# Optimization experiments

Hardware: AMD Instinct MI355X
Metric: run time of the kernel (lower is better)

## Reference

```python
import jax, jax.numpy as jnp
import numpy as np

N, E = 100000, 1600000
IN, H, OUT = 64, 64, 32
BN_EPS = 1e-5


def setup_inputs() -> dict:
    key = jax.random.key(0)
    ks = jax.random.split(key, 13)

    def w(k, shape, fan_in):
        return jax.random.uniform(k, shape, jnp.float32, -1.0, 1.0) / np.sqrt(fan_in)

    return {
        "x": jax.random.normal(ks[0], (N, IN), jnp.float32),
        "edge_index": jax.random.randint(ks[1], (2, E), 0, N, jnp.int32),
        "W1": w(ks[2], (IN, H), IN),
        "b1": jnp.zeros((H,), jnp.float32),
        "gamma": jnp.ones((H,), jnp.float32),
        "beta": jnp.zeros((H,), jnp.float32),
        "W2": w(ks[3], (H, H), H),
        "b2": jnp.zeros((H,), jnp.float32),
        "lin2_w": w(ks[4], (H, OUT), H),
        "lin2_b": w(ks[5], (OUT,), H),
        "lin3_w": w(ks[6], (OUT, H), OUT),
        "lin3_b": w(ks[7], (H,), OUT),
    }


def gcn_conv(x, src, dst, W, b):
    # PyG GCNConv: h = D^{-1/2} (A + I) D^{-1/2} (x W) + b
    n = x.shape[0]
    h = x @ W  # [N, H]
    loop = jnp.arange(n, dtype=src.dtype)
    s = jnp.concatenate([src, loop])  # add self-loops
    d = jnp.concatenate([dst, loop])
    deg = jax.ops.segment_sum(jnp.ones_like(s, x.dtype), d, num_segments=n)
    dinv = jnp.where(deg > 0, jax.lax.rsqrt(deg), 0.0)
    norm = dinv[s] * dinv[d]  # [E+N]
    msg = h[s] * norm[:, None]  # gather + scale
    out = jax.ops.segment_sum(msg, d, num_segments=n)  # scatter-add
    return out + b


def reference(x, edge_index, W1, b1, gamma, beta, W2, b2, lin2_w, lin2_b, lin3_w, lin3_b):
    src, dst = edge_index[0], edge_index[1]
    h = gcn_conv(x, src, dst, W1, b1)
    # BatchNorm1d in eval mode with default running stats (mean=0, var=1)
    h = gamma * (h * jax.lax.rsqrt(jnp.float32(1.0 + BN_EPS))) + beta
    h = jax.nn.relu(h)  # dropout is identity in eval
    h = gcn_conv(h, src, dst, W2, b2)
    logits = h @ lin2_w + lin2_b  # [N, OUT]
    p = jax.nn.softmax(logits, axis=-1)
    ent = -jnp.sum(p * jnp.log(p + 1e-9), axis=-1)  # [N]
    wts = 1.0 / (ent + 1e-10)
    wts = (wts - wts.min()) / (wts.max() - wts.min())
    wts = jax.nn.softmax(wts, axis=0)  # [N]
    graph = jnp.sum(logits * wts[:, None], axis=0, keepdims=True)  # [1, OUT]
    return graph @ lin3_w + lin3_b  # [1, H]
```

## Files before the change

### kernel.cpp

```cpp
#include <hip/hip_runtime.h>
#include <hip/hip_bf16.h>
#include <hip/hip_fp8.h>
#include <math.h>


#define F 64
#define OUTF 32
#define PB 128
#define LEDGE 5632
#define WG 512
#define BN_INV 0.9999950000374997f
#define ESC_X 32.0f
#define IESC_X 0.03125f
#define ESC_Z 64.0f
#define IESC_Z 0.015625f

typedef short bf16x8 __attribute__((ext_vector_type(8)));
typedef float f32x4 __attribute__((ext_vector_type(4)));

__device__ __forceinline__ unsigned short f2bf(float f) {
    unsigned u = __float_as_uint(f);
    return (unsigned short)((u + 0x7fffu + ((u >> 16) & 1u)) >> 16);
}
__device__ __forceinline__ float bf2f(unsigned short h) {
    return __uint_as_float((unsigned)h << 16);
}

#if __has_builtin(__builtin_amdgcn_cvt_f32_fp8) && __has_builtin(__builtin_amdgcn_cvt_pk_fp8_f32)
__device__ __forceinline__ float4 fp8x4(unsigned v) {
    return make_float4(__builtin_amdgcn_cvt_f32_fp8((int)v, 0),
                       __builtin_amdgcn_cvt_f32_fp8((int)v, 1),
                       __builtin_amdgcn_cvt_f32_fp8((int)v, 2),
                       __builtin_amdgcn_cvt_f32_fp8((int)v, 3));
}
__device__ __forceinline__ unsigned fp8pk4(float a, float b, float c, float d) {
    int r = __builtin_amdgcn_cvt_pk_fp8_f32(a, b, 0, false);
    r = __builtin_amdgcn_cvt_pk_fp8_f32(c, d, r, true);
    return (unsigned)r;
}
__device__ __forceinline__ unsigned char fp8enc1(float a) {
    return (unsigned char)(__builtin_amdgcn_cvt_pk_fp8_f32(a, a, 0, false) & 0xff);
}
#else
__device__ __forceinline__ float fp8d1(unsigned char b) {
    __hip_fp8_e4m3 v; v.__x = (__hip_fp8_storage_t)b; return (float)v;
}
__device__ __forceinline__ float4 fp8x4(unsigned v) {
    return make_float4(fp8d1(v & 255u), fp8d1((v >> 8) & 255u), fp8d1((v >> 16) & 255u), fp8d1((v >> 24) & 255u));
}
__device__ __forceinline__ unsigned char fp8enc1(float a) {
    return (unsigned char)__hip_fp8_e4m3(a).__x;
}
__device__ __forceinline__ unsigned fp8pk4(float a, float b, float c, float d) {
    return (unsigned)fp8enc1(a) | ((unsigned)fp8enc1(b) << 8) | ((unsigned)fp8enc1(c) << 16) | ((unsigned)fp8enc1(d) << 24);
}
#endif

__global__ __launch_bounds__(256) void k_hist(const int* __restrict__ dst, int* __restrict__ hist,
                                              int E, int NBK,
                                              const float* __restrict__ W1, const float* __restrict__ b1,
                                              const float* __restrict__ gamma, const float* __restrict__ beta,
                                              const float* __restrict__ W2, const float* __restrict__ b2,
                                              const float* __restrict__ l2w, const float* __restrict__ l2b,
                                              unsigned short* __restrict__ w1f, unsigned short* __restrict__ w2f,
                                              float* __restrict__ bias1f, float* __restrict__ b2l2) {
    __shared__ int lh[512];
    int t = threadIdx.x, blk = blockIdx.x;
    if (blk >= PB) {
        int tt = (blk - PB) * 256 + t;
        int k = tt >> 5, cc = tt & 31;
        float o = 0.0f;
        for (int j = 0; j < F; j++) o += W2[k * F + j] * l2w[j * OUTF + cc];
        {
            int t2 = cc >> 4, s = k >> 5, kb = (k >> 3) & 3, jj = k & 7;
            int ln = kb * 16 + (cc & 15);
            w2f[(size_t)((t2 * 2 + s) * 64 + ln) * 8 + jj] = f2bf(o);
        }
        for (int e = tt; e < F * F; e += 2048) {
            int kk = e >> 6, c = e & 63;
            float wv = W1[kk * F + c] * gamma[c] * BN_INV;
            int t1i = c >> 4, s = kk >> 5, kb = (kk >> 3) & 3, jj = kk & 7;
            int ln = kb * 16 + (c & 15);
            w1f[(size_t)((t1i * 2 + s) * 64 + ln) * 8 + jj] = f2bf(wv);
        }
        if (tt < F) bias1f[tt] = fmaf(b1[tt], gamma[tt] * BN_INV, beta[tt]);
        if (tt < OUTF) {
            float b = l2b[tt];
            for (int j = 0; j < F; j++) b += b2[j] * l2w[j * OUTF + tt];
            b2l2[tt] = b;
        }
        return;
    }
    for (int b = t; b < NBK; b += 256) lh[b] = 0;
    __syncthreads();
    int chunk = (E + PB - 1) / PB;
    int beg = blk * chunk, end = min(beg + chunk, E);
    for (int e = beg + t; e < end; e += 256) atomicAdd(&lh[dst[e] >> 8], 1);
    __syncthreads();
    for (int b = t; b < NBK; b += 256) hist[blk * NBK + b] = lh[b];
}

__global__ __launch_bounds__(PB) void k_hscan1(int* __restrict__ hist, int* __restrict__ btot, int NBK) {
    __shared__ int s[PB];
    int b = blockIdx.x, t = threadIdx.x;
    int v = hist[t * NBK + b];
    s[t] = v;
    __syncthreads();
    for (int off = 1; off < PB; off <<= 1) {
        int u = (t >= off) ? s[t - off] : 0;
        __syncthreads();
        s[t] += u;
        __syncthreads();
    }
    hist[t * NBK + b] = s[t] - v;
    if (t == PB - 1) btot[b] = s[t];
}

__global__ void k_hscan2(const int* __restrict__ btot, int* __restrict__ bbase, int NBK) {
    __shared__ int s[512];
    int t = threadIdx.x;
    int v = (t < NBK) ? btot[t] : 0;
    s[t] = v;
    __syncthreads();
    for (int off = 1; off < 512; off <<= 1) {
        int u = (t >= off) ? s[t - off] : 0;
        __syncthreads();
        s[t] += u;
        __syncthreads();
    }
    if (t < NBK) {
        bbase[t] = s[t] - v;
        if (t == NBK - 1) bbase[NBK] = s[t];
    }
}

__global__ __launch_bounds__(256) void k_place(const int* __restrict__ src, const int* __restrict__ dst,
                                               const int* __restrict__ hist, const int* __restrict__ bbase,
                                               unsigned* __restrict__ bucketArr, int E, int NBK) {
    __shared__ int cur[512];
    int t = threadIdx.x, blk = blockIdx.x;
    for (int b = t; b < NBK; b += 256) cur[b] = hist[blk * NBK + b] + bbase[b];
    __syncthreads();
    int chunk = (E + PB - 1) / PB;
    int beg = blk * chunk, end = min(beg + chunk, E);
    for (int e = beg + t; e < end; e += 256) {
        int d = dst[e], sidx = src[e];
        int p = atomicAdd(&cur[d >> 8], 1);
        bucketArr[p] = ((unsigned)sidx << 8) | (unsigned)(d & 255);
    }
}

__global__ __launch_bounds__(256) void k_binsort(const unsigned* __restrict__ bucketArr,
                                                 const int* __restrict__ bbase,
                                                 int* __restrict__ eidx, int4* __restrict__ meta,
                                                 const float4* __restrict__ x4, unsigned* __restrict__ xq, int N) {
    __shared__ unsigned ledge[LEDGE];
    __shared__ int lcnt[256], lofs[256], lcur[256], lscan[256];
    __shared__ float ldinv[256];
    int b = blockIdx.x, t = threadIdx.x;
    int gb = bbase[b];
    int count = min(bbase[b + 1] - gb, LEDGE);
    for (int j = t; j < count; j += 256) ledge[j] = bucketArr[gb + j];
    lcnt[t] = 0;
    __syncthreads();
    for (int j = t; j < count; j += 256) atomicAdd(&lcnt[ledge[j] & 255u], 1);
    __syncthreads();
    int deg = lcnt[t];
    lscan[t] = deg;
    __syncthreads();
    for (int off = 1; off < 256; off <<= 1) {
        int u = (t >= off) ? lscan[t - off] : 0;
        __syncthreads();
        lscan[t] += u;
        __syncthreads();
    }
    lofs[t] = lscan[t] - deg;
    lcur[t] = 0;
    int node = (b << 8) + t;
    float di = rsqrtf((float)deg + 1.0f);
    ldinv[t] = di;
    if (node < N) meta[node] = make_int4(gb + lofs[t], deg, __float_as_int(di), 0);
    __syncthreads();
    for (int j = t; j < count; j += 256) {
        unsigned v = ledge[j];
        int loc = (int)(v & 255u);
        int p = atomicAdd(&lcur[loc], 1);
        eidx[gb + lofs[loc] + p] = (int)(v >> 8);
    }
    for (int idx = t; idx < 256 * 16; idx += 256) {
        int nd = (b << 8) + (idx >> 4);
        if (nd < N) {
            float d2 = ldinv[idx >> 4] * ESC_X;
            float4 v = x4[(size_t)nd * 16 + (idx & 15)];
            xq[(size_t)nd * 16 + (idx & 15)] = fp8pk4(v.x * d2, v.y * d2, v.z * d2, v.w * d2);
        }
    }
}

__device__ __forceinline__ void conv1_consume(const uint2 (&vbuf)[24], uint2 selfv, int dcnt,
                                              int i, int beg, float dis, int gl, int gbase,
                                              const uint2* __restrict__ xq2, const int* __restrict__ eidx,
                                              int Em1, unsigned short* __restrict__ t1, int N) {
    float4 aA0 = fp8x4(selfv.x), aB0 = fp8x4(selfv.y);
    float4 aA1 = make_float4(0.f, 0.f, 0.f, 0.f), aB1 = aA1;
#pragma unroll
    for (int k = 0; k < 24; k++) {
        if (k < dcnt) {
            float4 vA = fp8x4(vbuf[k].x), vB = fp8x4(vbuf[k].y);
            if (k & 1) {
                aA1.x += vA.x; aA1.y += vA.y; aA1.z += vA.z; aA1.w += vA.w;
                aB1.x += vB.x; aB1.y += vB.y; aB1.z += vB.z; aB1.w += vB.w;
            } else {
                aA0.x += vA.x; aA0.y += vA.y; aA0.z += vA.z; aA0.w += vA.w;
                aB0.x += vB.x; aB0.y += vB.y; aB0.z += vB.z; aB0.w += vB.w;
            }
        }
    }
    for (int base = 24; base < dcnt; base += 8) {
        int j = base + gl;
        int ss = eidx[min(beg + j, Em1)];
        int cnt = min(dcnt - base, 8);
#pragma unroll
        for (int k = 0; k < 8; k++) {
            if (k < cnt) {
                int sv = __shfl(ss, gbase + k, 64);
                uint2 v = xq2[(size_t)sv * 8 + gl];
                float4 vA = fp8x4(v.x), vB = fp8x4(v.y);
                aA0.x += vA.x; aA0.y += vA.y; aA0.z += vA.z; aA0.w += vA.w;
                aB0.x += vB.x; aB0.y += vB.y; aB0.z += vB.z; aB0.w += vB.w;
            }
        }
    }
    if (i < N) {
        float4 oA, oB;
        oA.x = (aA0.x + aA1.x) * dis; oA.y = (aA0.y + aA1.y) * dis;
        oA.z = (aA0.z + aA1.z) * dis; oA.w = (aA0.w + aA1.w) * dis;
        oB.x = (aB0.x + aB1.x) * dis; oB.y = (aB0.y + aB1.y) * dis;
        oB.z = (aB0.z + aB1.z) * dis; oB.w = (aB0.w + aB1.w) * dis;
        uint4 ob;
        ob.x = (unsigned)f2bf(oA.x) | ((unsigned)f2bf(oA.y) << 16);
        ob.y = (unsigned)f2bf(oA.z) | ((unsigned)f2bf(oA.w) << 16);
        ob.z = (unsigned)f2bf(oB.x) | ((unsigned)f2bf(oB.y) << 16);
        ob.w = (unsigned)f2bf(oB.z) | ((unsigned)f2bf(oB.w) << 16);
        *(uint4*)(t1 + (size_t)i * F + gl * 8) = ob;
    }
}

__global__ __launch_bounds__(256, 2) void k_conv1agg(const uint2* __restrict__ xq2,
                                                     const int4* __restrict__ meta,
                                                     const int* __restrict__ eidx,
                                                     unsigned short* __restrict__ t1, int N, int Em1) {
    int tid = threadIdx.x, wave = tid >> 6, lane = tid & 63;
    int g = lane >> 3, gl = lane & 7, gbase = lane & 56;
    int wgid = blockIdx.x * 4 + wave;
    int i0 = wgid * 16 + g;
    int i1 = wgid * 16 + 8 + g;
    int i0c = min(i0, N - 1), i1c = min(i1, N - 1);
    int4 m0 = meta[i0c], m1 = meta[i1c];
    int beg0 = m0.x, beg1 = m1.x;
    int d0 = (i0 < N) ? m0.y : 0;
    int d1 = (i1 < N) ? m1.y : 0;
    float dis0 = __int_as_float(m0.z) * IESC_X;
    float dis1 = __int_as_float(m1.z) * IESC_X;
    int sA0 = eidx[min(beg0 + gl, Em1)];
    int sA1 = eidx[min(beg0 + 8 + gl, Em1)];
    int sA2 = eidx[min(beg0 + 16 + gl, Em1)];
    int sB0 = eidx[min(beg1 + gl, Em1)];
    int sB1 = eidx[min(beg1 + 8 + gl, Em1)];
    int sB2 = eidx[min(beg1 + 16 + gl, Em1)];
    uint2 self0 = xq2[(size_t)i0c * 8 + gl];
    uint2 self1 = xq2[(size_t)i1c * 8 + gl];
    uint2 vb0[24], vb1[24];
#pragma unroll
    for (int k = 0; k < 24; k++) {
        int sreg = (k < 8) ? sA0 : (k < 16) ? sA1 : sA2;
        int sv = __shfl(sreg, gbase + (k & 7), 64);
        sv = (k < d0) ? sv : i0c;
        vb0[k] = xq2[(size_t)sv * 8 + gl];
    }
#pragma unroll
    for (int k = 0; k < 24; k++) {
        int sreg = (k < 8) ? sB0 : (k < 16) ? sB1 : sB2;
        int sv = __shfl(sreg, gbase + (k & 7), 64);
        sv = (k < d1) ? sv : i1c;
        vb1[k] = xq2[(size_t)sv * 8 + gl];
    }
    __builtin_amdgcn_sched_barrier(0);
    conv1_consume(vb0, self0, d0, i0, beg0, dis0, gl, gbase, xq2, eidx, Em1, t1, N);
    conv1_consume(vb1, self1, d1, i1, beg1, dis1, gl, gbase, xq2, eidx, Em1, t1, N);
}

__global__ __launch_bounds__(256) void k_zm(const unsigned short* __restrict__ t1bf,
                                            const int4* __restrict__ meta,
                                            const unsigned short* __restrict__ w1f,
                                            const unsigned short* __restrict__ w2f,
                                            const float* __restrict__ bias1f,
                                            unsigned char* __restrict__ z2q, int N) {
    __shared__ __align__(16) unsigned short hlds[4][16][72];
    __shared__ float ldin[4][16];
    int tid = threadIdx.x, wave = tid >> 6, lane = tid & 63;
    int cl = lane & 15, kb = lane >> 4;
    int ntiles = (N + 15) >> 4;
    int tile = blockIdx.x * 4 + wave;
    if (tile >= ntiles) return;
    int row0 = tile << 4;

    int ra = min(row0 + cl, N - 1);
    const bf16x8* arow = (const bf16x8*)(t1bf + (size_t)ra * F);
    bf16x8 a0 = arow[kb];
    bf16x8 a1 = arow[4 + kb];
    if (lane < 16) ldin[wave][lane] = __int_as_float(meta[min(row0 + lane, N - 1)].z);

    const bf16x8* w1v = (const bf16x8*)w1f;
    const bf16x8* w2v = (const bf16x8*)w2f;
    bf16x8 w1frag[8];
#pragma unroll
    for (int q = 0; q < 8; q++) w1frag[q] = w1v[q * 64 + lane];
    bf16x8 w2frag[4];
#pragma unroll
    for (int q = 0; q < 4; q++) w2frag[q] = w2v[q * 64 + lane];
    float bias_t[4];
#pragma unroll
    for (int t = 0; t < 4; t++) bias_t[t] = bias1f[t * 16 + cl];

    f32x4 acc[4] = {};
#pragma unroll
    for (int t = 0; t < 4; t++) {
        acc[t] = __builtin_amdgcn_mfma_f32_16x16x32_bf16(a0, w1frag[t * 2 + 0], acc[t], 0, 0, 0);
        acc[t] = __builtin_amdgcn_mfma_f32_16x16x32_bf16(a1, w1frag[t * 2 + 1], acc[t], 0, 0, 0);
    }
    float di[4];
#pragma unroll
    for (int j = 0; j < 4; j++) di[j] = ldin[wave][kb * 4 + j];
#pragma unroll
    for (int t = 0; t < 4; t++)
#pragma unroll
        for (int j = 0; j < 4; j++) {
            float h = fmaxf(acc[t][j] + bias_t[t], 0.0f) * di[j];
            hlds[wave][kb * 4 + j][t * 16 + cl] = f2bf(h);
        }
    bf16x8 h0 = *(const bf16x8*)&hlds[wave][cl][kb * 8];
    bf16x8 h1 = *(const bf16x8*)&hlds[wave][cl][32 + kb * 8];
    f32x4 accz[2] = {};
#pragma unroll
    for (int t2 = 0; t2 < 2; t2++) {
        accz[t2] = __builtin_amdgcn_mfma_f32_16x16x32_bf16(h0, w2frag[t2 * 2 + 0], accz[t2], 0, 0, 0);
        accz[t2] = __builtin_amdgcn_mfma_f32_16x16x32_bf16(h1, w2frag[t2 * 2 + 1], accz[t2], 0, 0, 0);
    }
#pragma unroll
    for (int t2 = 0; t2 < 2; t2++)
#pragma unroll
        for (int j = 0; j < 4; j++) {
            int r = row0 + kb * 4 + j;
            if (r < N) z2q[(size_t)r * OUTF + t2 * 16 + cl] = fp8enc1(accz[t2][j] * ESC_Z);
        }
}

__device__ __forceinline__ void conv2_consume(const uint2 (&vbuf)[24], uint2 selfv, int dcnt,
                                              int i, int beg, float dis, int gl, int gbase,
                                              const uint2* __restrict__ z2q2, const int* __restrict__ eidx,
                                              int Em1, float4 bvA, float4 bvB,
                                              unsigned short* __restrict__ logits_bf,
                                              float* __restrict__ wraw,
                                              float& mnW, float& mxW, int N) {
    float4 aA0 = fp8x4(selfv.x), aB0 = fp8x4(selfv.y);
    if (i >= N) { aA0 = make_float4(0.f, 0.f, 0.f, 0.f); aB0 = aA0; }
    float4 aA1 = make_float4(0.f, 0.f, 0.f, 0.f), aB1 = aA1;
#pragma unroll
    for (int k = 0; k < 24; k++) {
        if (k < dcnt) {
            float4 vA = fp8x4(vbuf[k].x), vB = fp8x4(vbuf[k].y);
            if (k & 1) {
                aA1.x += vA.x; aA1.y += vA.y; aA1.z += vA.z; aA1.w += vA.w;
                aB1.x += vB.x; aB1.y += vB.y; aB1.z += vB.z; aB1.w += vB.w;
            } else {
                aA0.x += vA.x; aA0.y += vA.y; aA0.z += vA.z; aA0.w += vA.w;
                aB0.x += vB.x; aB0.y += vB.y; aB0.z += vB.z; aB0.w += vB.w;
            }
        }
    }
    for (int base = 24; base < dcnt; base += 4) {
        int j = base + gl;
        int ss = eidx[min(beg + j, Em1)];
        int cnt = min(dcnt - base, 4);
#pragma unroll
        for (int k = 0; k < 4; k++) {
            if (k < cnt) {
                int sv = __shfl(ss, gbase + k, 64);
                uint2 v = z2q2[(size_t)sv * 4 + gl];
                float4 vA = fp8x4(v.x), vB = fp8x4(v.y);
                aA0.x += vA.x; aA0.y += vA.y; aA0.z += vA.z; aA0.w += vA.w;
                aB0.x += vB.x; aB0.y += vB.y; aB0.z += vB.z; aB0.w += vB.w;
            }
        }
    }
    float4 lgA, lgB;
    lgA.x = fmaf(aA0.x + aA1.x, dis, bvA.x);
    lgA.y = fmaf(aA0.y + aA1.y, dis, bvA.y);
    lgA.z = fmaf(aA0.z + aA1.z, dis, bvA.z);
    lgA.w = fmaf(aA0.w + aA1.w, dis, bvA.w);
    lgB.x = fmaf(aB0.x + aB1.x, dis, bvB.x);
    lgB.y = fmaf(aB0.y + aB1.y, dis, bvB.y);
    lgB.z = fmaf(aB0.z + aB1.z, dis, bvB.z);
    lgB.w = fmaf(aB0.w + aB1.w, dis, bvB.w);
    if (i < N) {
        uint4 ob;
        ob.x = (unsigned)f2bf(lgA.x) | ((unsigned)f2bf(lgA.y) << 16);
        ob.y = (unsigned)f2bf(lgA.z) | ((unsigned)f2bf(lgA.w) << 16);
        ob.z = (unsigned)f2bf(lgB.x) | ((unsigned)f2bf(lgB.y) << 16);
        ob.w = (unsigned)f2bf(lgB.z) | ((unsigned)f2bf(lgB.w) << 16);
        *(uint4*)(logits_bf + (size_t)i * OUTF + gl * 8) = ob;
    }
    float m8 = fmaxf(fmaxf(fmaxf(lgA.x, lgA.y), fmaxf(lgA.z, lgA.w)),
                     fmaxf(fmaxf(lgB.x, lgB.y), fmaxf(lgB.z, lgB.w)));
    for (int off = 2; off > 0; off >>= 1) m8 = fmaxf(m8, __shfl_xor(m8, off, 4));
    float p0 = __expf(lgA.x - m8), p1 = __expf(lgA.y - m8), p2 = __expf(lgA.z - m8), p3 = __expf(lgA.w - m8);
    float p4 = __expf(lgB.x - m8), p5 = __expf(lgB.y - m8), p6 = __expf(lgB.z - m8), p7 = __expf(lgB.w - m8);
    float s8 = p0 + p1 + p2 + p3 + p4 + p5 + p6 + p7;
    for (int off = 2; off > 0; off >>= 1) s8 += __shfl_xor(s8, off, 4);
    float inv = 1.0f / s8;
    float t0 = p0 * inv, t1v = p1 * inv, t2v = p2 * inv, t3 = p3 * inv;
    float t4 = p4 * inv, t5 = p5 * inv, t6 = p6 * inv, t7 = p7 * inv;
    float e8 = t0 * __logf(t0 + 1e-9f) + t1v * __logf(t1v + 1e-9f) + t2v * __logf(t2v + 1e-9f) + t3 * __logf(t3 + 1e-9f) +
               t4 * __logf(t4 + 1e-9f) + t5 * __logf(t5 + 1e-9f) + t6 * __logf(t6 + 1e-9f) + t7 * __logf(t7 + 1e-9f);
    for (int off = 2; off > 0; off >>= 1) e8 += __shfl_xor(e8, off, 4);
    float w = 1.0f / (-e8 + 1e-10f);
    if (i < N) {
        if (gl == 0) wraw[i] = w;
        mnW = fminf(mnW, w);
        mxW = fmaxf(mxW, w);
    }
}

__global__ __launch_bounds__(256, 2) void k_conv2agg(const uint2* __restrict__ z2q2,
                                                     const int4* __restrict__ meta,
                                                     const int* __restrict__ eidx, const float* __restrict__ b2l2,
                                                     unsigned short* __restrict__ logits_bf, float* __restrict__ wraw,
                                                     float* __restrict__ mnmx, int N, int Em1) {
    __shared__ float smn[4], smx[4];
    int tid = threadIdx.x, wave = tid >> 6, lane = tid & 63;
    int g = lane >> 2, gl = lane & 3, gbase = lane & 60;
    float4 bvA = ((const float4*)b2l2)[gl * 2];
    float4 bvB = ((const float4*)b2l2)[gl * 2 + 1];
    int wgid = blockIdx.x * 4 + wave;
    int i0 = wgid * 32 + g;
    int i1 = wgid * 32 + 16 + g;
    int i0c = min(i0, N - 1), i1c = min(i1, N - 1);
    int4 m0 = meta[i0c], m1 = meta[i1c];
    int beg0 = m0.x, beg1 = m1.x;
    int d0 = (i0 < N) ? m0.y : 0;
    int d1 = (i1 < N) ? m1.y : 0;
    float dis0 = __int_as_float(m0.z) * IESC_Z;
    float dis1 = __int_as_float(m1.z) * IESC_Z;
    int sA0 = eidx[min(beg0 + gl, Em1)];
    int sA1 = eidx[min(beg0 + 4 + gl, Em1)];
    int sA2 = eidx[min(beg0 + 8 + gl, Em1)];
    int sA3 = eidx[min(beg0 + 12 + gl, Em1)];
    int sA4 = eidx[min(beg0 + 16 + gl, Em1)];
    int sA5 = eidx[min(beg0 + 20 + gl, Em1)];
    int sB0 = eidx[min(beg1 + gl, Em1)];
    int sB1 = eidx[min(beg1 + 4 + gl, Em1)];
    int sB2 = eidx[min(beg1 + 8 + gl, Em1)];
    int sB3 = eidx[min(beg1 + 12 + gl, Em1)];
    int sB4 = eidx[min(beg1 + 16 + gl, Em1)];
    int sB5 = eidx[min(beg1 + 20 + gl, Em1)];
    uint2 self0 = z2q2[(size_t)i0c * 4 + gl];
    uint2 self1 = z2q2[(size_t)i1c * 4 + gl];
    uint2 vb0[24], vb1[24];
#pragma unroll
    for (int k = 0; k < 24; k++) {
        int sreg = (k < 4) ? sA0 : (k < 8) ? sA1 : (k < 12) ? sA2 : (k < 16) ? sA3 : (k < 20) ? sA4 : sA5;
        int sv = __shfl(sreg, gbase + (k & 3), 64);
        sv = (k < d0) ? sv : i0c;
        vb0[k] = z2q2[(size_t)sv * 4 + gl];
    }
#pragma unroll
    for (int k = 0; k < 24; k++) {
        int sreg = (k < 4) ? sB0 : (k < 8) ? sB1 : (k < 12) ? sB2 : (k < 16) ? sB3 : (k < 20) ? sB4 : sB5;
        int sv = __shfl(sreg, gbase + (k & 3), 64);
        sv = (k < d1) ? sv : i1c;
        vb1[k] = z2q2[(size_t)sv * 4 + gl];
    }
    __builtin_amdgcn_sched_barrier(0);
    float mnW = INFINITY, mxW = -INFINITY;
    conv2_consume(vb0, self0, d0, i0, beg0, dis0, gl, gbase, z2q2, eidx, Em1,
                  bvA, bvB, logits_bf, wraw, mnW, mxW, N);
    conv2_consume(vb1, self1, d1, i1, beg1, dis1, gl, gbase, z2q2, eidx, Em1,
                  bvA, bvB, logits_bf, wraw, mnW, mxW, N);
    for (int off = 32; off > 0; off >>= 1) {
        mnW = fminf(mnW, __shfl_xor(mnW, off, 64));
        mxW = fmaxf(mxW, __shfl_xor(mxW, off, 64));
    }
    if (lane == 0) { smn[wave] = mnW; smx[wave] = mxW; }
    __syncthreads();
    if (tid == 0) {
        mnmx[blockIdx.x * 2]     = fminf(fminf(smn[0], smn[1]), fminf(smn[2], smn[3]));
        mnmx[blockIdx.x * 2 + 1] = fmaxf(fmaxf(smx[0], smx[1]), fmaxf(smx[2], smx[3]));
    }
}

__global__ __launch_bounds__(256) void k_weight(const unsigned short* __restrict__ logits_bf,
                                                const float* __restrict__ wraw,
                                                const float* __restrict__ mnmx, int nmm,
                                                float* __restrict__ part, int N) {
    __shared__ float rmn[4], rmx[4];
    float mn = INFINITY, mx = -INFINITY;
    for (int j = threadIdx.x; j < nmm; j += 256) {
        mn = fminf(mn, mnmx[j * 2]);
        mx = fmaxf(mx, mnmx[j * 2 + 1]);
    }
    for (int off = 32; off > 0; off >>= 1) {
        mn = fminf(mn, __shfl_xor(mn, off, 64));
        mx = fmaxf(mx, __shfl_xor(mx, off, 64));
    }
    int wv = threadIdx.x >> 6;
    if ((threadIdx.x & 63) == 0) { rmn[wv] = mn; rmx[wv] = mx; }
    __syncthreads();
    mn = fminf(fminf(rmn[0], rmn[1]), fminf(rmn[2], rmn[3]));
    mx = fmaxf(fmaxf(rmx[0], rmx[1]), fmaxf(rmx[2], rmx[3]));
    float inv = 1.0f / (mx - mn);
    int c = threadIdx.x & 31;
    int g = threadIdx.x >> 5;
    float acc = 0.0f, es = 0.0f;
    for (int r = blockIdx.x * 8 + g; r < N; r += gridDim.x * 8) {
        float e = __expf((wraw[r] - mn) * inv);
        acc += e * bf2f(logits_bf[(size_t)r * OUTF + c]);
        if (c == 0) es += e;
    }
    __shared__ float sa[8][OUTF];
    __shared__ float se[8];
    sa[g][c] = acc;
    if (c == 0) se[g] = es;
    __syncthreads();
    if (g == 0) {
        float t = sa[0][c];
#pragma unroll
        for (int i = 1; i < 8; i++) t += sa[i][c];
        part[blockIdx.x * 36 + c] = t;
        if (c == 0) {
            float u = 0.0f;
#pragma unroll
            for (int i = 0; i < 8; i++) u += se[i];
            part[blockIdx.x * 36 + 32] = u;
        }
    }
}

__global__ __launch_bounds__(256) void k_final(const float* __restrict__ part,
                                               const float* __restrict__ w3, const float* __restrict__ b3,
                                               float* __restrict__ out) {
    __shared__ float sa[8][OUTF];
    __shared__ float se[8];
    __shared__ float facc[OUTF + 1];
    int tid = threadIdx.x;
    int g = tid >> 5, c = tid & 31;
    float acc = 0.0f, es = 0.0f;
    for (int p = g; p < WG; p += 8) {
        acc += part[p * 36 + c];
        if (c == 0) es += part[p * 36 + 32];
    }
    sa[g][c] = acc;
    if (c == 0) se[g] = es;
    __syncthreads();
    if (tid < OUTF) {
        float t = 0.0f;
#pragma unroll
        for (int i = 0; i < 8; i++) t += sa[i][tid];
        facc[tid] = t;
    }
    if (tid == 32) {
        float u = 0.0f;
#pragma unroll
        for (int i = 0; i < 8; i++) u += se[i];
        facc[OUTF] = u;
    }
    __syncthreads();
    if (tid < F) {
        float s = facc[OUTF];
        float o = b3[tid];
#pragma unroll
        for (int cc = 0; cc < OUTF; cc++) o += (facc[cc] / s) * w3[cc * F + tid];
        out[tid] = o;
    }
}

extern "C" void kernel_launch(void* const* d_in, const int* in_sizes, int n_in,
                              void* d_out, int out_size, void* d_ws, size_t ws_size,
                              hipStream_t stream) {
    const float* x     = (const float*)d_in[0];
    const int*   ei    = (const int*)d_in[1];
    const float* W1    = (const float*)d_in[2];
    const float* b1    = (const float*)d_in[3];
    const float* gamma = (const float*)d_in[4];
    const float* beta  = (const float*)d_in[5];
    const float* W2    = (const float*)d_in[6];
    const float* b2    = (const float*)d_in[7];
    const float* l2w   = (const float*)d_in[8];
    const float* l2b   = (const float*)d_in[9];
    const float* l3w   = (const float*)d_in[10];
    const float* l3b   = (const float*)d_in[11];

    int N = in_sizes[0] / F;
    int E = in_sizes[1] / 2;
    const int* src = ei;
    const int* dst = ei + E;
    int NBK = (N + 255) >> 8;

    char* p = (char*)d_ws;
    int* hist = (int*)p;                p += (size_t)PB * NBK * 4;
    int* btot = (int*)p;                p += 512 * 4;
    int* bbase = (int*)p;               p += 516 * 4;
    unsigned* bucketArr = (unsigned*)p; p += (size_t)E * 4;
    int4* meta = (int4*)p;              p += (size_t)N * 16;
    int* eidx = (int*)p;                p += (size_t)E * 4;
    float* mnmx = (float*)p;            p += 2048 * 4;
    float* part = (float*)p;            p += (size_t)WG * 36 * 4;
    unsigned short* w1f = (unsigned short*)p;  p += F * F * 2;
    unsigned short* w2f = (unsigned short*)p;  p += F * OUTF * 2;
    float* bias1f = (float*)p;          p += F * 4;
    float* b2l2 = (float*)p;            p += OUTF * 4 + 32;
    unsigned* xq = (unsigned*)p;        p += (size_t)N * F;
    unsigned short* t1bf = (unsigned short*)p; p += (size_t)N * F * 2;
    float* wraw = (float*)p;            p += (size_t)N * 4;
    unsigned char* z2q = (unsigned char*)xq;
    unsigned short* logits_bf = (unsigned short*)t1bf;

    k_hist<<<PB + 8, 256, 0, stream>>>(dst, hist, E, NBK, W1, b1, gamma, beta, W2, b2, l2w, l2b,
                                       w1f, w2f, bias1f, b2l2);
    k_hscan1<<<NBK, PB, 0, stream>>>(hist, btot, NBK);
    k_hscan2<<<1, 512, 0, stream>>>(btot, bbase, NBK);
    k_place<<<PB, 256, 0, stream>>>(src, dst, hist, bbase, bucketArr, E, NBK);
    k_binsort<<<NBK, 256, 0, stream>>>(bucketArr, bbase, eidx, meta, (const float4*)x, xq, N);

    int nb1 = (N + 63) / 64;
    k_conv1agg<<<nb1, 256, 0, stream>>>((const uint2*)xq, meta, eidx, t1bf, N, E - 1);
    int nt = (N + 15) >> 4;
    k_zm<<<(nt + 3) / 4, 256, 0, stream>>>(t1bf, meta, w1f, w2f, bias1f, z2q, N);
    int wg2 = (nt + 1) >> 1;
    int nb2 = (wg2 + 3) >> 2;
    k_conv2agg<<<nb2, 256, 0, stream>>>((const uint2*)z2q, meta, eidx, b2l2, logits_bf, wraw, mnmx, N, E - 1);

    k_weight<<<WG, 256, 0, stream>>>(logits_bf, wraw, mnmx, nb2, part, N);
    k_final<<<1, 256, 0, stream>>>(part, l3w, l3b, (float*)d_out);
}
```

Baseline: 244.5 us.

## Split fp8 feature table into two column halves for conv1 aggregation

```diff
diff --git a/kernel.cpp b/kernel.cpp
--- a/kernel.cpp
+++ b/kernel.cpp
@@ -191,16 +191,19 @@
         int nd = (b << 8) + (idx >> 4);
         if (nd < N) {
             float d2 = ldinv[idx >> 4] * ESC_X;
-            float4 v = x4[(size_t)nd * 16 + (idx & 15)];
-            xq[(size_t)nd * 16 + (idx & 15)] = fp8pk4(v.x * d2, v.y * d2, v.z * d2, v.w * d2);
-        }
-    }
-}
-
-__device__ __forceinline__ void conv1_consume(const uint2 (&vbuf)[24], uint2 selfv, int dcnt,
-                                              int i, int beg, float dis, int gl, int gbase,
-                                              const uint2* __restrict__ xq2, const int* __restrict__ eidx,
-                                              int Em1, unsigned short* __restrict__ t1, int N) {
+            int w = idx & 15;
+            int h = w >> 3, wq = w & 7;
+            float4 v = x4[(size_t)nd * 16 + w];
+            xq[((size_t)h * N + nd) * 8 + wq] = fp8pk4(v.x * d2, v.y * d2, v.z * d2, v.w * d2);
+        }
+    }
+}
+
+__device__ __forceinline__ void conv1h_consume(const uint2 (&vbuf)[24], uint2 selfv, int dcnt,
+                                               int i, int beg, float dis, int gl, int gbase,
+                                               const uint2* __restrict__ xqh2, size_t hN,
+                                               const int* __restrict__ eidx, int Em1, int h,
+                                               unsigned short* __restrict__ t1, int N) {
     float4 aA0 = fp8x4(selfv.x), aB0 = fp8x4(selfv.y);
     float4 aA1 = make_float4(0.f, 0.f, 0.f, 0.f), aB1 = aA1;
 #pragma unroll
@@ -216,15 +219,15 @@
             }
         }
     }
-    for (int base = 24; base < dcnt; base += 8) {
+    for (int base = 24; base < dcnt; base += 4) {
         int j = base + gl;
         int ss = eidx[min(beg + j, Em1)];
-        int cnt = min(dcnt - base, 8);
-#pragma unroll
-        for (int k = 0; k < 8; k++) {
+        int cnt = min(dcnt - base, 4);
+#pragma unroll
+        for (int k = 0; k < 4; k++) {
             if (k < cnt) {
                 int sv = __shfl(ss, gbase + k, 64);
-                uint2 v = xq2[(size_t)sv * 8 + gl];
+                uint2 v = xqh2[(hN + (size_t)sv) * 4 + gl];
                 float4 vA = fp8x4(v.x), vB = fp8x4(v.y);
                 aA0.x += vA.x; aA0.y += vA.y; aA0.z += vA.z; aA0.w += vA.w;
                 aB0.x += vB.x; aB0.y += vB.y; aB0.z += vB.z; aB0.w += vB.w;
@@ -242,19 +245,22 @@
         ob.y = (unsigned)f2bf(oA.z) | ((unsigned)f2bf(oA.w) << 16);
         ob.z = (unsigned)f2bf(oB.x) | ((unsigned)f2bf(oB.y) << 16);
         ob.w = (unsigned)f2bf(oB.z) | ((unsigned)f2bf(oB.w) << 16);
-        *(uint4*)(t1 + (size_t)i * F + gl * 8) = ob;
-    }
-}
-
-__global__ __launch_bounds__(256, 2) void k_conv1agg(const uint2* __restrict__ xq2,
-                                                     const int4* __restrict__ meta,
-                                                     const int* __restrict__ eidx,
-                                                     unsigned short* __restrict__ t1, int N, int Em1) {
+        *(uint4*)(t1 + (size_t)i * F + h * 32 + gl * 8) = ob;
+    }
+}
+
+__global__ __launch_bounds__(256, 2) void k_conv1h(const uint2* __restrict__ xqh2,
+                                                   const int4* __restrict__ meta,
+                                                   const int* __restrict__ eidx,
+                                                   unsigned short* __restrict__ t1, int N, int Em1) {
     int tid = threadIdx.x, wave = tid >> 6, lane = tid & 63;
-    int g = lane >> 3, gl = lane & 7, gbase = lane & 56;
-    int wgid = blockIdx.x * 4 + wave;
-    int i0 = wgid * 16 + g;
-    int i1 = wgid * 16 + 8 + g;
+    int g = lane >> 2, gl = lane & 3, gbase = lane & 60;
+    int h = blockIdx.x & 1;
+    size_t hN = (size_t)h * N;
+    int pb = blockIdx.x >> 1;
+    int wgid = pb * 4 + wave;
+    int i0 = wgid * 32 + g;
+    int i1 = wgid * 32 + 16 + g;
     int i0c = min(i0, N - 1), i1c = min(i1, N - 1);
     int4 m0 = meta[i0c], m1 = meta[i1c];
     int beg0 = m0.x, beg1 = m1.x;
@@ -263,31 +269,37 @@
     float dis0 = __int_as_float(m0.z) * IESC_X;
     float dis1 = __int_as_float(m1.z) * IESC_X;
     int sA0 = eidx[min(beg0 + gl, Em1)];
-    int sA1 = eidx[min(beg0 + 8 + gl, Em1)];
-    int sA2 = eidx[min(beg0 + 16 + gl, Em1)];
+    int sA1 = eidx[min(beg0 + 4 + gl, Em1)];
+    int sA2 = eidx[min(beg0 + 8 + gl, Em1)];
+    int sA3 = eidx[min(beg0 + 12 + gl, Em1)];
+    int sA4 = eidx[min(beg0 + 16 + gl, Em1)];
+    int sA5 = eidx[min(beg0 + 20 + gl, Em1)];
     int sB0 = eidx[min(beg1 + gl, Em1)];
-    int sB1 = eidx[min(beg1 + 8 + gl, Em1)];
-    int sB2 = eidx[min(beg1 + 16 + gl, Em1)];
-    uint2 self0 = xq2[(size_t)i0c * 8 + gl];
-    uint2 self1 = xq2[(size_t)i1c * 8 + gl];
+    int sB1 = eidx[min(beg1 + 4 + gl, Em1)];
+    int sB2 = eidx[min(beg1 + 8 + gl, Em1)];
+    int sB3 = eidx[min(beg1 + 12 + gl, Em1)];
+    int sB4 = eidx[min(beg1 + 16 + gl, Em1)];
+    int sB5 = eidx[min(beg1 + 20 + gl, Em1)];
+    uint2 self0 = xqh2[(hN + (size_t)i0c) * 4 + gl];
+    uint2 self1 = xqh2[(hN + (size_t)i1c) * 4 + gl];
     uint2 vb0[24], vb1[24];
 #pragma unroll
     for (int k = 0; k < 24; k++) {
-        int sreg = (k < 8) ? sA0 : (k < 16) ? sA1 : sA2;
-        int sv = __shfl(sreg, gbase + (k & 7), 64);
+        int sreg = (k < 4) ? sA0 : (k < 8) ? sA1 : (k < 12) ? sA2 : (k < 16) ? sA3 : (k < 20) ? sA4 : sA5;
+        int sv = __shfl(sreg, gbase + (k & 3), 64);
         sv = (k < d0) ? sv : i0c;
-        vb0[k] = xq2[(size_t)sv * 8 + gl];
+        vb0[k] = xqh2[(hN + (size_t)sv) * 4 + gl];
     }
 #pragma unroll
     for (int k = 0; k < 24; k++) {
-        int sreg = (k < 8) ? sB0 : (k < 16) ? sB1 : sB2;
-        int sv = __shfl(sreg, gbase + (k & 7), 64);
+        int sreg = (k < 4) ? sB0 : (k < 8) ? sB1 : (k < 12) ? sB2 : (k < 16) ? sB3 : (k < 20) ? sB4 : sB5;
+        int sv = __shfl(sreg, gbase + (k & 3), 64);
         sv = (k < d1) ? sv : i1c;
-        vb1[k] = xq2[(size_t)sv * 8 + gl];
+        vb1[k] = xqh2[(hN + (size_t)sv) * 4 + gl];
     }
     __builtin_amdgcn_sched_barrier(0);
-    conv1_consume(vb0, self0, d0, i0, beg0, dis0, gl, gbase, xq2, eidx, Em1, t1, N);
-    conv1_consume(vb1, self1, d1, i1, beg1, dis1, gl, gbase, xq2, eidx, Em1, t1, N);
+    conv1h_consume(vb0, self0, d0, i0, beg0, dis0, gl, gbase, xqh2, hN, eidx, Em1, h, t1, N);
+    conv1h_consume(vb1, self1, d1, i1, beg1, dis1, gl, gbase, xqh2, hN, eidx, Em1, h, t1, N);
 }
 
 __global__ __launch_bounds__(256) void k_zm(const unsigned short* __restrict__ t1bf,
@@ -632,8 +644,8 @@
     k_place<<<PB, 256, 0, stream>>>(src, dst, hist, bbase, bucketArr, E, NBK);
     k_binsort<<<NBK, 256, 0, stream>>>(bucketArr, bbase, eidx, meta, (const float4*)x, xq, N);
 
-    int nb1 = (N + 63) / 64;
-    k_conv1agg<<<nb1, 256, 0, stream>>>((const uint2*)xq, meta, eidx, t1bf, N, E - 1);
+    int nbw = (N + 127) / 128;
+    k_conv1h<<<nbw * 2, 256, 0, stream>>>((const uint2*)xq, meta, eidx, t1bf, N, E - 1);
     int nt = (N + 15) >> 4;
     k_zm<<<(nt + 3) / 4, 256, 0, stream>>>(t1bf, meta, w1f, w2f, bias1f, z2q, N);
     int wg2 = (nt + 1) >> 1;
```

After: 242.3 us. No clear change (-0.9%).
